# Kernel optimization log

Hardware: AMD Instinct MI355X
Metric: run time of the kernel (lower is better)

## Reference

```python
import jax, jax.numpy as jnp
import numpy as np

B, LOC_MAX, MAX_LEN, EMB, D_DELTA = 16, 20000, 100, 256, 2


def setup_inputs() -> dict:
    key = jax.random.key(0)
    k1, k2, k3, k4, k5 = jax.random.split(key, 5)
    return {
        "self_attn": jax.random.normal(k1, (B, MAX_LEN, EMB), dtype=jnp.float32),
        "self_delta": jax.random.uniform(k2, (B, MAX_LEN, LOC_MAX, D_DELTA), dtype=jnp.float32),
        "traj_len": jax.random.randint(k3, (B,), 0, MAX_LEN, dtype=jnp.int64),
        "emb_table": jax.random.normal(k4, (LOC_MAX + 1, EMB), dtype=jnp.float32) * 0.02,
        "value_w": jax.random.normal(k5, (1, MAX_LEN), dtype=jnp.float32) * 0.1,
    }


def reference(self_attn, self_delta, traj_len, emb_table, value_w):
    # self_delta: [B, max_len, loc_max, D] -> sum last dim -> [B, max_len, loc_max]
    # -> transpose(-1, -2) -> [B, loc_max, max_len]
    delta = jnp.swapaxes(jnp.sum(self_delta, axis=-1), -1, -2)
    loc_max = emb_table.shape[0] - 1
    # candidates = arange(1, loc_max+1) is batch-invariant -> single gather slice
    emb_cand = emb_table[1:loc_max + 1]  # [loc_max, emb]
    # bmm(emb_candidates, self_attn^T): [B, loc_max, max_len], fused with delta mul
    attn = jnp.einsum('le,bme->blm', emb_cand, self_attn) * delta
    # Linear(max_len, 1, bias=False) -> reduce over max_len -> [B, loc_max]
    attn_out = jnp.einsum('blm,m->bl', attn, value_w[0])
    return attn_out
```

## Files before the change

### kernel.cpp

```cpp
#include <hip/hip_runtime.h>

#define NB 16
#define MLEN 100
#define EMBD 256
#define LMAX 20000
#define LTILE 64
#define NLT 313
#define NKC 4
#define FSTRIDE 520
#define PREP_TASKS (NB * NKC * 16 * 64)

typedef __attribute__((ext_vector_type(4))) float f32x4;
typedef __attribute__((ext_vector_type(2))) float f32x2;
typedef _Float16 f16x8 __attribute__((ext_vector_type(8)));

__device__ __forceinline__ unsigned short f2h(float x) {
    union { _Float16 f; unsigned short u; } a; a.f = (_Float16)x; return a.u;
}

__global__ __launch_bounds__(256)
void prep2_kernel(const float* __restrict__ attn, const float* __restrict__ vw,
                  unsigned short* __restrict__ Bf) {
    const int gid  = blockIdx.x * 256 + threadIdx.x;
    const int lane = gid & 63;
    const int f    = gid >> 6;
    const int etg  = f & 15;
    const int kcb  = f >> 4;
    const int kc   = kcb & 3;
    const int b    = kcb >> 2;
    const int e    = etg * 16 + (lane & 15);
    const int m0   = kc * 32 + (lane >> 4) * 8;
    unsigned h[8];
    #pragma unroll
    for (int j = 0; j < 8; ++j) {
        const int m = m0 + j;
        float x = 0.f;
        if (m < MLEN) x = vw[m] * attn[((size_t)b * MLEN + m) * EMBD + e];
        h[j] = f2h(x);
    }
    uint4 hi = make_uint4(h[0]|(h[1]<<16), h[2]|(h[3]<<16), h[4]|(h[5]<<16), h[6]|(h[7]<<16));
    reinterpret_cast<uint4*>(Bf)[gid] = hi;
}

__global__ __launch_bounds__(256, 3)
void main_kernel(const unsigned short* __restrict__ Bf,
                 const float* __restrict__ sdelta, const float* __restrict__ embt,
                 float* __restrict__ out) {
    __shared__ __align__(16) unsigned short AhL[2][4 * FSTRIDE];
    __shared__ float red[256];

    const int b    = blockIdx.x;
    const int lt0  = blockIdx.y;
    const int l0   = lt0 * LTILE;
    const int w    = threadIdx.x >> 6;
    const int lane = threadIdx.x & 63;
    const int llo  = lane & 15;
    const int lhi  = lane >> 4;

    f32x4 acc[4][4];
    #pragma unroll
    for (int lt = 0; lt < 4; ++lt)
        #pragma unroll
        for (int et = 0; et < 4; ++et)
            acc[lt][et] = (f32x4){0.f, 0.f, 0.f, 0.f};

    const int lcl = min(l0 + lane, LMAX - 1);

    f32x2 vA[2][8];
    auto issueA = [&](int kc) {
        const int q = kc & 1;
        #pragma unroll
        for (int jj = 0; jj < 8; ++jj) {
            const int m  = kc * 32 + jj * 4 + w;
            const int mc = (m < MLEN) ? m : (MLEN - 1);
            vA[q][jj] = *reinterpret_cast<const f32x2*>(
                            sdelta + ((size_t)(b * MLEN + mc) * LMAX + lcl) * 2);
        }
    };
    auto writeA = [&](int kc) {
        const int q  = kc & 1;
        const int lt = lane >> 4;
        const int ll = lane & 15;
        #pragma unroll
        for (int jj = 0; jj < 8; ++jj) {
            const int r32 = jj * 4 + w;
            const int m   = kc * 32 + r32;
            const float msk = (m < MLEN) ? 1.f : 0.f;
            const f32x2 v = vA[q][jj];
            const int kg = r32 >> 3, j = r32 & 7;
            AhL[q][lt * FSTRIDE + (ll | (kg << 4)) * 8 + j] = f2h((v[0] + v[1]) * msk);
        }
    };
    auto loadB = [&](int kc, f16x8* dst) {
        #pragma unroll
        for (int et = 0; et < 4; ++et) {
            const size_t bo = (((size_t)(b * NKC + kc) * 16 + (w * 4 + et)) * 64 + lane) * 8;
            dst[et] = *reinterpret_cast<const f16x8*>(Bf + bo);
        }
    };

    f16x8 Bc[4], Bn[4];
    issueA(0);
    loadB(0, Bc);
    #pragma unroll
    for (int kc = 0; kc < NKC; ++kc) {
        const int q = kc & 1;
        writeA(kc);
        asm volatile("s_waitcnt lgkmcnt(0)" ::: "memory");
        __builtin_amdgcn_sched_barrier(0);
        __builtin_amdgcn_s_barrier();
        __builtin_amdgcn_sched_barrier(0);

        if (kc + 1 < NKC) {
            issueA(kc + 1);
            loadB(kc + 1, Bn);
        }
        __builtin_amdgcn_sched_barrier(0);

        #pragma unroll
        for (int lt = 0; lt < 4; ++lt) {
            const f16x8 ah = *reinterpret_cast<const f16x8*>(&AhL[q][lt * FSTRIDE + lane * 8]);
            #pragma unroll
            for (int et = 0; et < 4; ++et)
                acc[lt][et] = __builtin_amdgcn_mfma_f32_16x16x32_f16(ah, Bc[et], acc[lt][et], 0, 0, 0);
        }
        if (kc + 1 < NKC) { Bc[0] = Bn[0]; Bc[1] = Bn[1]; Bc[2] = Bn[2]; Bc[3] = Bn[3]; }
    }

    float p[4][4];
    #pragma unroll
    for (int lt = 0; lt < 4; ++lt) {
        #pragma unroll
        for (int i = 0; i < 4; ++i) {
            const int l  = l0 + lt * 16 + lhi * 4 + i;
            const int lc = (l < LMAX) ? l : (LMAX - 1);
            const float* Er = embt + (size_t)(1 + lc) * EMBD + w * 64 + llo;
            float s = acc[lt][0][i] * Er[0];
            s += acc[lt][1][i] * Er[16];
            s += acc[lt][2][i] * Er[32];
            s += acc[lt][3][i] * Er[48];
            p[lt][i] = s;
        }
    }
    #pragma unroll
    for (int lt = 0; lt < 4; ++lt)
        #pragma unroll
        for (int i = 0; i < 4; ++i) {
            float x = p[lt][i];
            x += __shfl_xor(x, 1);
            x += __shfl_xor(x, 2);
            x += __shfl_xor(x, 4);
            x += __shfl_xor(x, 8);
            p[lt][i] = x;
        }
    if (llo == 0) {
        #pragma unroll
        for (int lt = 0; lt < 4; ++lt)
            *reinterpret_cast<float4*>(&red[w * 64 + lt * 16 + lhi * 4]) =
                make_float4(p[lt][0], p[lt][1], p[lt][2], p[lt][3]);
    }
    __syncthreads();
    if (threadIdx.x < 64) {
        const int t = threadIdx.x;
        const int l = l0 + t;
        if (l < LMAX) {
            out[(size_t)b * LMAX + l] = red[t] + red[64 + t] + red[128 + t] + red[192 + t];
        }
    }
}

__global__ __launch_bounds__(256)
void fallback_kernel(const float* __restrict__ attn, const float* __restrict__ sdelta,
                     const float* __restrict__ embt, const float* __restrict__ vw,
                     float* __restrict__ out) {
    const int idx = blockIdx.x * 256 + threadIdx.x;
    if (idx >= NB * LMAX) return;
    const int b = idx / LMAX;
    const int l = idx % LMAX;
    float s = 0.f;
    for (int m = 0; m < MLEN; ++m) {
        const float* ar = attn + ((size_t)b * MLEN + m) * EMBD;
        const float* er = embt + (size_t)(l + 1) * EMBD;
        float dot = 0.f;
        for (int e = 0; e < EMBD; ++e) dot += ar[e] * er[e];
        const size_t so = (((size_t)b * MLEN + m) * LMAX + l) * 2;
        s += dot * vw[m] * (sdelta[so] + sdelta[so + 1]);
    }
    out[idx] = s;
}

extern "C" void kernel_launch(void* const* d_in, const int* in_sizes, int n_in,
                              void* d_out, int out_size, void* d_ws, size_t ws_size,
                              hipStream_t stream) {
    const float* attn   = (const float*)d_in[0];
    const float* sdelta = (const float*)d_in[1];
    const float* embt   = (const float*)d_in[3];
    const float* vw     = (const float*)d_in[4];
    float* out = (float*)d_out;

    const size_t fragShorts = (size_t)PREP_TASKS * 8;
    const size_t needed     = fragShorts * sizeof(unsigned short);

    if (ws_size >= needed) {
        unsigned short* Bf = (unsigned short*)d_ws;
        prep2_kernel<<<PREP_TASKS / 256, 256, 0, stream>>>(attn, vw, Bf);
        main_kernel<<<dim3(NB, NLT), 256, 0, stream>>>(Bf, sdelta, embt, out);
    } else {
        fallback_kernel<<<(NB * LMAX + 255) / 256, 256, 0, stream>>>(attn, sdelta, embt, vw, out);
    }
}
```

Measured before the change: 77.59 us.

## Stage delta and B fragments via direct global-to-LDS loads with two-chunk prefetch

```diff
diff --git a/kernel.cpp b/kernel.cpp
--- a/kernel.cpp
+++ b/kernel.cpp
@@ -7,12 +7,12 @@
 #define LTILE 64
 #define NLT 313
 #define NKC 4
-#define FSTRIDE 520
 #define PREP_TASKS (NB * NKC * 16 * 64)
 
 typedef __attribute__((ext_vector_type(4))) float f32x4;
-typedef __attribute__((ext_vector_type(2))) float f32x2;
 typedef _Float16 f16x8 __attribute__((ext_vector_type(8)));
+typedef const __attribute__((address_space(1))) unsigned int* as1_u32p;
+typedef __attribute__((address_space(3))) unsigned int* as3_u32p;
 
 __device__ __forceinline__ unsigned short f2h(float x) {
     union { _Float16 f; unsigned short u; } a; a.f = (_Float16)x; return a.u;
@@ -42,11 +42,12 @@
     reinterpret_cast<uint4*>(Bf)[gid] = hi;
 }
 
-__global__ __launch_bounds__(256, 3)
+__global__ __launch_bounds__(256, 2)
 void main_kernel(const unsigned short* __restrict__ Bf,
                  const float* __restrict__ sdelta, const float* __restrict__ embt,
                  float* __restrict__ out) {
-    __shared__ __align__(16) unsigned short AhL[2][4 * FSTRIDE];
+    __shared__ __align__(16) char SD[2][32 * 512];
+    __shared__ __align__(16) char BL[2][16 * 1024];
     __shared__ float red[256];
 
     const int b    = blockIdx.x;
@@ -64,67 +65,76 @@
         for (int et = 0; et < 4; ++et)
             acc[lt][et] = (f32x4){0.f, 0.f, 0.f, 0.f};
 
-    const int lcl = min(l0 + lane, LMAX - 1);
-
-    f32x2 vA[2][8];
-    auto issueA = [&](int kc) {
+    const int rhalf = lane >> 5;
+    const int lp    = lane & 31;
+    const int lcl   = min(l0 + 2 * lp, LMAX - 2);
+
+    auto stageChunk = [&](int kc) {
         const int q = kc & 1;
         #pragma unroll
-        for (int jj = 0; jj < 8; ++jj) {
-            const int m  = kc * 32 + jj * 4 + w;
-            const int mc = (m < MLEN) ? m : (MLEN - 1);
-            vA[q][jj] = *reinterpret_cast<const f32x2*>(
-                            sdelta + ((size_t)(b * MLEN + mc) * LMAX + lcl) * 2);
+        for (int jj = 0; jj < 4; ++jj) {
+            const int j = w + 4 * jj;
+            const int m = kc * 32 + 2 * j + rhalf;
+            const float* src = sdelta + ((size_t)(b * MLEN + min(m, MLEN - 1)) * LMAX + lcl) * 2;
+            char* dst = &SD[q][j * 1024];
+            __builtin_amdgcn_global_load_lds((as1_u32p)(const void*)src,
+                                             (as3_u32p)(void*)dst, 16, 0, 0);
+        }
+        #pragma unroll
+        for (int jj = 0; jj < 4; ++jj) {
+            const int floc = w + 4 * jj;
+            const unsigned short* src = Bf + (((size_t)(b * NKC + kc) * 16 + floc) * 64 + lane) * 8;
+            char* dst = &BL[q][floc * 1024];
+            __builtin_amdgcn_global_load_lds((as1_u32p)(const void*)src,
+                                             (as3_u32p)(void*)dst, 16, 0, 0);
         }
     };
-    auto writeA = [&](int kc) {
-        const int q  = kc & 1;
-        const int lt = lane >> 4;
-        const int ll = lane & 15;
-        #pragma unroll
-        for (int jj = 0; jj < 8; ++jj) {
-            const int r32 = jj * 4 + w;
-            const int m   = kc * 32 + r32;
-            const float msk = (m < MLEN) ? 1.f : 0.f;
-            const f32x2 v = vA[q][jj];
-            const int kg = r32 >> 3, j = r32 & 7;
-            AhL[q][lt * FSTRIDE + (ll | (kg << 4)) * 8 + j] = f2h((v[0] + v[1]) * msk);
-        }
-    };
-    auto loadB = [&](int kc, f16x8* dst) {
-        #pragma unroll
-        for (int et = 0; et < 4; ++et) {
-            const size_t bo = (((size_t)(b * NKC + kc) * 16 + (w * 4 + et)) * 64 + lane) * 8;
-            dst[et] = *reinterpret_cast<const f16x8*>(Bf + bo);
-        }
-    };
-
-    f16x8 Bc[4], Bn[4];
-    issueA(0);
-    loadB(0, Bc);
+
+    stageChunk(0);
+    stageChunk(1);
+
     #pragma unroll
     for (int kc = 0; kc < NKC; ++kc) {
         const int q = kc & 1;
-        writeA(kc);
-        asm volatile("s_waitcnt lgkmcnt(0)" ::: "memory");
+        __builtin_amdgcn_sched_barrier(0);
+        if (kc < NKC - 1) asm volatile("s_waitcnt vmcnt(8)" ::: "memory");
+        else              asm volatile("s_waitcnt vmcnt(0)" ::: "memory");
         __builtin_amdgcn_sched_barrier(0);
         __builtin_amdgcn_s_barrier();
         __builtin_amdgcn_sched_barrier(0);
 
-        if (kc + 1 < NKC) {
-            issueA(kc + 1);
-            loadB(kc + 1, Bn);
-        }
-        __builtin_amdgcn_sched_barrier(0);
+        f16x8 bb[4];
+        #pragma unroll
+        for (int et = 0; et < 4; ++et)
+            bb[et] = *reinterpret_cast<const f16x8*>(&BL[q][(w * 4 + et) * 1024 + lane * 16]);
 
         #pragma unroll
         for (int lt = 0; lt < 4; ++lt) {
-            const f16x8 ah = *reinterpret_cast<const f16x8*>(&AhL[q][lt * FSTRIDE + lane * 8]);
+            const int base = (lt * 16 + llo) * 8;
+            float2 vv[8];
+            #pragma unroll
+            for (int j = 0; j < 8; ++j)
+                vv[j] = *reinterpret_cast<const float2*>(&SD[q][(lhi * 8 + j) * 512 + base]);
+            unsigned u[4];
+            #pragma unroll
+            for (int jp = 0; jp < 4; ++jp) {
+                const int mg = kc * 32 + lhi * 8 + 2 * jp;
+                const float s0 = (mg     < MLEN) ? (vv[2 * jp].x + vv[2 * jp].y) : 0.f;
+                const float s1 = (mg + 1 < MLEN) ? (vv[2 * jp + 1].x + vv[2 * jp + 1].y) : 0.f;
+                u[jp] = (unsigned)f2h(s0) | ((unsigned)f2h(s1) << 16);
+            }
+            union { uint4 ui; f16x8 v; } ac;
+            ac.ui = make_uint4(u[0], u[1], u[2], u[3]);
             #pragma unroll
             for (int et = 0; et < 4; ++et)
-                acc[lt][et] = __builtin_amdgcn_mfma_f32_16x16x32_f16(ah, Bc[et], acc[lt][et], 0, 0, 0);
-        }
-        if (kc + 1 < NKC) { Bc[0] = Bn[0]; Bc[1] = Bn[1]; Bc[2] = Bn[2]; Bc[3] = Bn[3]; }
+                acc[lt][et] = __builtin_amdgcn_mfma_f32_16x16x32_f16(ac.v, bb[et], acc[lt][et], 0, 0, 0);
+        }
+
+        __builtin_amdgcn_sched_barrier(0);
+        __builtin_amdgcn_s_barrier();
+        __builtin_amdgcn_sched_barrier(0);
+        if (kc + 2 < NKC) stageChunk(kc + 2);
+        __builtin_amdgcn_sched_barrier(0);
     }
 
     float p[4][4];
```

New measurement: 99.06 us. 1.28x slower.

## Issue all delta loads up front with two 64-row K chunks and vectorized LDS writes

Applied to the files above, without the earlier changes.

```diff
diff --git a/kernel.cpp b/kernel.cpp
--- a/kernel.cpp
+++ b/kernel.cpp
@@ -6,9 +6,7 @@
 #define LMAX 20000
 #define LTILE 64
 #define NLT 313
-#define NKC 4
-#define FSTRIDE 520
-#define PREP_TASKS (NB * NKC * 16 * 64)
+#define PREP_TASKS (NB * 4 * 16 * 64)
 
 typedef __attribute__((ext_vector_type(4))) float f32x4;
 typedef __attribute__((ext_vector_type(2))) float f32x2;
@@ -26,10 +24,10 @@
     const int f    = gid >> 6;
     const int etg  = f & 15;
     const int kcb  = f >> 4;
-    const int kc   = kcb & 3;
+    const int kc4  = kcb & 3;
     const int b    = kcb >> 2;
     const int e    = etg * 16 + (lane & 15);
-    const int m0   = kc * 32 + (lane >> 4) * 8;
+    const int m0   = kc4 * 32 + (lane >> 4) * 8;
     unsigned h[8];
     #pragma unroll
     for (int j = 0; j < 8; ++j) {
@@ -42,11 +40,11 @@
     reinterpret_cast<uint4*>(Bf)[gid] = hi;
 }
 
-__global__ __launch_bounds__(256, 3)
+__global__ __launch_bounds__(256, 2)
 void main_kernel(const unsigned short* __restrict__ Bf,
                  const float* __restrict__ sdelta, const float* __restrict__ embt,
                  float* __restrict__ out) {
-    __shared__ __align__(16) unsigned short AhL[2][4 * FSTRIDE];
+    __shared__ __align__(16) unsigned short AhL[2][4 * 1040];
     __shared__ float red[256];
 
     const int b    = blockIdx.x;
@@ -65,66 +63,74 @@
             acc[lt][et] = (f32x4){0.f, 0.f, 0.f, 0.f};
 
     const int lcl = min(l0 + lane, LMAX - 1);
-
-    f32x2 vA[2][8];
+    const float* sdb = sdelta + (size_t)b * MLEN * (LMAX * 2);
+
+    f32x2 vA[2][16];
     auto issueA = [&](int kc) {
         const int q = kc & 1;
         #pragma unroll
-        for (int jj = 0; jj < 8; ++jj) {
-            const int m  = kc * 32 + jj * 4 + w;
+        for (int jj = 0; jj < 16; ++jj) {
+            const int m  = kc * 64 + w * 16 + jj;
             const int mc = (m < MLEN) ? m : (MLEN - 1);
-            vA[q][jj] = *reinterpret_cast<const f32x2*>(
-                            sdelta + ((size_t)(b * MLEN + mc) * LMAX + lcl) * 2);
+            vA[q][jj] = *reinterpret_cast<const f32x2*>(sdb + (size_t)mc * (LMAX * 2) + lcl * 2);
         }
     };
     auto writeA = [&](int kc) {
         const int q  = kc & 1;
         const int lt = lane >> 4;
         const int ll = lane & 15;
-        #pragma unroll
-        for (int jj = 0; jj < 8; ++jj) {
-            const int r32 = jj * 4 + w;
-            const int m   = kc * 32 + r32;
-            const float msk = (m < MLEN) ? 1.f : 0.f;
-            const f32x2 v = vA[q][jj];
-            const int kg = r32 >> 3, j = r32 & 7;
-            AhL[q][lt * FSTRIDE + (ll | (kg << 4)) * 8 + j] = f2h((v[0] + v[1]) * msk);
+        const int ks = w >> 1;
+        #pragma unroll
+        for (int g = 0; g < 2; ++g) {
+            const int kgrp = (w & 1) * 2 + g;
+            unsigned h[8];
+            #pragma unroll
+            for (int j = 0; j < 8; ++j) {
+                const int m = kc * 64 + w * 16 + g * 8 + j;
+                const float msk = (m < MLEN) ? 1.f : 0.f;
+                const f32x2 v = vA[q][g * 8 + j];
+                h[j] = f2h((v[0] + v[1]) * msk);
+            }
+            const int i0 = lt * 1040 + ks * 520 + (ll | (kgrp << 4)) * 8;
+            *reinterpret_cast<uint4*>(&AhL[q][i0]) =
+                make_uint4(h[0]|(h[1]<<16), h[2]|(h[3]<<16), h[4]|(h[5]<<16), h[6]|(h[7]<<16));
         }
     };
-    auto loadB = [&](int kc, f16x8* dst) {
-        #pragma unroll
-        for (int et = 0; et < 4; ++et) {
-            const size_t bo = (((size_t)(b * NKC + kc) * 16 + (w * 4 + et)) * 64 + lane) * 8;
-            dst[et] = *reinterpret_cast<const f16x8*>(Bf + bo);
-        }
-    };
-
-    f16x8 Bc[4], Bn[4];
+
     issueA(0);
-    loadB(0, Bc);
-    #pragma unroll
-    for (int kc = 0; kc < NKC; ++kc) {
+    issueA(1);
+    f16x8 Bv[2][2][4];
+    #pragma unroll
+    for (int kc = 0; kc < 2; ++kc)
+        #pragma unroll
+        for (int ks = 0; ks < 2; ++ks)
+            #pragma unroll
+            for (int et = 0; et < 4; ++et) {
+                const int kc4 = kc * 2 + ks;
+                const size_t bo = (((size_t)(b * 4 + kc4) * 16 + (w * 4 + et)) * 64 + lane) * 8;
+                Bv[kc][ks][et] = *reinterpret_cast<const f16x8*>(Bf + bo);
+            }
+
+    #pragma unroll
+    for (int kc = 0; kc < 2; ++kc) {
         const int q = kc & 1;
         writeA(kc);
+        __builtin_amdgcn_sched_barrier(0);
         asm volatile("s_waitcnt lgkmcnt(0)" ::: "memory");
         __builtin_amdgcn_sched_barrier(0);
         __builtin_amdgcn_s_barrier();
         __builtin_amdgcn_sched_barrier(0);
 
-        if (kc + 1 < NKC) {
-            issueA(kc + 1);
-            loadB(kc + 1, Bn);
-        }
-        __builtin_amdgcn_sched_barrier(0);
-
         #pragma unroll
         for (int lt = 0; lt < 4; ++lt) {
-            const f16x8 ah = *reinterpret_cast<const f16x8*>(&AhL[q][lt * FSTRIDE + lane * 8]);
             #pragma unroll
-            for (int et = 0; et < 4; ++et)
-                acc[lt][et] = __builtin_amdgcn_mfma_f32_16x16x32_f16(ah, Bc[et], acc[lt][et], 0, 0, 0);
-        }
-        if (kc + 1 < NKC) { Bc[0] = Bn[0]; Bc[1] = Bn[1]; Bc[2] = Bn[2]; Bc[3] = Bn[3]; }
+            for (int ks = 0; ks < 2; ++ks) {
+                const f16x8 ah = *reinterpret_cast<const f16x8*>(&AhL[q][lt * 1040 + ks * 520 + lane * 8]);
+                #pragma unroll
+                for (int et = 0; et < 4; ++et)
+                    acc[lt][et] = __builtin_amdgcn_mfma_f32_16x16x32_f16(ah, Bv[kc][ks][et], acc[lt][et], 0, 0, 0);
+            }
+        }
     }
 
     float p[4][4];
```

After: 74.86 us. 1.04x faster.
